# Optimization experiments

Measured on AMD Instinct MI355X. Metric: run time of the kernel, lower is better.

The kernel has to match this reference:

```python
import jax, jax.numpy as jnp
import numpy as np

EPS = 1e-5
HEADS = 4
RES = 28          # resolution H = W
PS = 14           # patch_size (pooled grid side)
POOL = RES // PS  # patch_pool_size = 2


def _local_init_pos_w():
    # Deterministic local init (locality_strength=1.0); kernel_size = sqrt(num_heads) = 2
    ks = int(HEADS ** 0.5)
    center = (ks - 1) / 2 if ks % 2 == 0 else ks // 2
    w = np.zeros((HEADS, 3), dtype=np.float32)
    for h1 in range(ks):
        for h2 in range(ks):
            pos = h1 + ks * h2
            w[pos, 2] = -1.0
            w[pos, 1] = 2.0 * (h1 - center)
            w[pos, 0] = 2.0 * (h2 - center)
    return jnp.asarray(w)


def setup_inputs() -> dict:
    key = jax.random.key(0)
    B, T, C = 32, RES * RES, 768
    x = jax.random.normal(key, (B, T, C), dtype=jnp.float32)
    return {
        "x": x,
        "weight": jnp.ones((C,), jnp.float32),
        "bias": jnp.zeros((C,), jnp.float32),
        "mean_norm_weight": jnp.zeros((HEADS,), jnp.float32),
        "var_norm_weight": jnp.zeros((HEADS,), jnp.float32),
        "pos_w": _local_init_pos_w(),
        "pos_b": jnp.zeros((HEADS,), jnp.float32),
    }


def _rel_indices(ps, dtype):
    # (P, P, 3) relative position features: [indx, indy, indx^2 + indy^2]
    ind = jnp.arange(ps)[None, :] - jnp.arange(ps)[:, None]  # (ps, ps)
    indx = jnp.tile(ind, (ps, ps))                            # (P, P)
    indy = jnp.repeat(jnp.repeat(ind, ps, axis=0), ps, axis=1)
    return jnp.stack([indx, indy, indx * indx + indy * indy], axis=-1).astype(dtype)


def reference(x, weight, bias, mean_norm_weight, var_norm_weight, pos_w, pos_b):
    B, T, C = x.shape
    Ch = C // HEADS
    P = PS * PS

    # group "moment2" normalization
    g = x.reshape(B, T, HEADS, Ch)
    m2 = jnp.mean(g * g, axis=3, keepdims=True)
    xn = (g / jnp.sqrt(m2 + EPS)).reshape(B, T, C)

    mw = jax.nn.sigmoid(mean_norm_weight)  # (HEADS,)
    vw = jax.nn.sigmoid(var_norm_weight)

    # position scores: Linear(3 -> heads) then softmax over source-patch axis
    rel = _rel_indices(PS, x.dtype)                 # (P, P, 3)
    scores = rel @ pos_w.T + pos_b                  # (P, P, HEADS)
    pos = jax.nn.softmax(scores, axis=0)            # softmax over dim -2 of (B,h,i,j)
    pos_h = jnp.transpose(pos, (2, 0, 1))           # (HEADS, P, P)

    mean_ln = xn.mean(axis=2)                       # (B, T)
    var_ln = xn.var(axis=2, ddof=1)                 # torch unbiased var

    # spatialize + avg-pool POOLxPOOL
    xs = xn.reshape(B, RES, RES, C).transpose(0, 3, 1, 2)          # (B, C, 28, 28)
    xp = xs.reshape(B, C, PS, POOL, PS, POOL).mean(axis=(3, 5))    # (B, C, 14, 14)
    xp = xp.reshape(B, HEADS, Ch, P)

    mean_r = jnp.einsum('bhci,hij->bhcj', xp, pos_h)
    mean2_r = jnp.einsum('bhci,hij->bhcj', xp * xp, pos_h)
    var_r = mean2_r - mean_r * mean_r

    def unpool(y):  # nearest-neighbor upsample back to T tokens
        y = y.reshape(B, HEADS, Ch, PS, PS)
        y = jnp.broadcast_to(y[:, :, :, :, None, :, None],
                             (B, HEADS, Ch, PS, POOL, PS, POOL))
        return y.reshape(B, HEADS, Ch, T)

    mean_r = unpool(mean_r)
    var_r = unpool(var_r)

    mwv = mw.reshape(1, HEADS, 1, 1)
    vwv = vw.reshape(1, HEADS, 1, 1)
    mean_r = (1.0 - mwv) * mean_r + mwv * mean_ln[:, None, None, :]
    var_r = (1.0 - vwv) * var_r + vwv * var_ln[:, None, None, :]

    mean_r = mean_r.reshape(B, C, T).transpose(0, 2, 1)  # (B, T, C)
    var_r = var_r.reshape(B, C, T).transpose(0, 2, 1)

    out = (xn - mean_r) / jnp.sqrt(var_r + EPS)
    return out * weight.reshape(1, 1, C) + bias.reshape(1, 1, C)
```

## Files before the change

### kernel.cpp

```cpp
#include <hip/hip_runtime.h>

#define NB   32
#define NT   784
#define NC   768
#define NH   4
#define CH   192
#define PSZ  14
#define NP   196
#define RESO 28
#define EPSV 1e-5f
#define CSL  32
#define NSLC (NC / CSL)
#define BTH  448

__global__ __launch_bounds__(256) void k_norm_pool(
    const float* __restrict__ x,
    float* __restrict__ inv_m2, float* __restrict__ mean_ln,
    float* __restrict__ var_ln, float4* __restrict__ xp4) {
  __shared__ float4 xl4[4 * 192];
  int bid = blockIdx.x;
  int b = bid / NP, ip = bid % NP;
  int pr = ip / PSZ, pc = ip % PSZ;
  int tid = threadIdx.x;
  int k = tid >> 6, lane = tid & 63;
  int t = (2 * pr + (k >> 1)) * RESO + (2 * pc + (k & 1));

  const float4* row = (const float4*)(x + (size_t)(b * NT + t) * NC);
  int f4b = (lane >> 4) * 48 + (lane & 15) * 3;
  float4 v0 = row[f4b], v1 = row[f4b + 1], v2 = row[f4b + 2];

  float d = v0.x * v0.x + v0.y * v0.y + v0.z * v0.z + v0.w * v0.w +
            v1.x * v1.x + v1.y * v1.y + v1.z * v1.z + v1.w * v1.w +
            v2.x * v2.x + v2.y * v2.y + v2.z * v2.z + v2.w * v2.w;
#pragma unroll
  for (int s = 1; s <= 8; s <<= 1) d += __shfl_xor(d, s, 64);
  float iv = rsqrtf(d * (1.f / CH) + EPSV);
  if ((lane & 15) == 0)
    inv_m2[(size_t)(b * NT + t) * NH + (lane >> 4)] = iv;

  v0.x *= iv; v0.y *= iv; v0.z *= iv; v0.w *= iv;
  v1.x *= iv; v1.y *= iv; v1.z *= iv; v1.w *= iv;
  v2.x *= iv; v2.y *= iv; v2.z *= iv; v2.w *= iv;

  float sm = v0.x + v0.y + v0.z + v0.w + v1.x + v1.y + v1.z + v1.w +
             v2.x + v2.y + v2.z + v2.w;
  float sq = v0.x * v0.x + v0.y * v0.y + v0.z * v0.z + v0.w * v0.w +
             v1.x * v1.x + v1.y * v1.y + v1.z * v1.z + v1.w * v1.w +
             v2.x * v2.x + v2.y * v2.y + v2.z * v2.z + v2.w * v2.w;
#pragma unroll
  for (int s = 1; s <= 32; s <<= 1) {
    sm += __shfl_xor(sm, s, 64);
    sq += __shfl_xor(sq, s, 64);
  }
  if (lane == 0) {
    float mean = sm / (float)NC;
    mean_ln[b * NT + t] = mean;
    var_ln[b * NT + t] = (sq - (float)NC * mean * mean) / (float)(NC - 1);
  }

  xl4[k * 192 + f4b]     = v0;
  xl4[k * 192 + f4b + 1] = v1;
  xl4[k * 192 + f4b + 2] = v2;
  __syncthreads();

  if (tid < 192) {
    float4 a = xl4[tid], bb = xl4[192 + tid], c = xl4[384 + tid], dd = xl4[576 + tid];
    float4 r;
    r.x = (a.x + bb.x + c.x + dd.x) * 0.25f;
    r.y = (a.y + bb.y + c.y + dd.y) * 0.25f;
    r.z = (a.z + bb.z + c.z + dd.z) * 0.25f;
    r.w = (a.w + bb.w + c.w + dd.w) * 0.25f;
    xp4[(size_t)(b * NP + ip) * 192 + tid] = r;
  }
}

__global__ __launch_bounds__(BTH) void k_fused(
    const float4* __restrict__ xp4, const float* __restrict__ pos_w,
    const float* __restrict__ mnw, const float* __restrict__ vnw,
    const float* __restrict__ x,
    const float* __restrict__ weight, const float* __restrict__ bias,
    const float* __restrict__ inv_m2, const float* __restrict__ mean_ln,
    const float* __restrict__ var_ln, float* __restrict__ out) {
  __shared__ float4 sxp4[NP * (CSL / 4)];
  __shared__ float sF[PSZ * PSZ];
  __shared__ float sG[PSZ * PSZ];
  __shared__ float tstat[NT][3];

  int bid0 = blockIdx.x;
  int bidS = (bid0 & 7) * 96 + (bid0 >> 3);
  int b = bidS / NSLC, s = bidS % NSLC;
  int hs = s / 6;
  int tid = threadIdx.x;
  int jx = tid >> 5;
  int ch = tid & 31;
  int c = s * CSL + ch;

  if (tid < PSZ) {
    int jf = tid;
    float w0 = pos_w[hs * 3 + 0], w2 = pos_w[hs * 3 + 2];
    float e[PSZ], mx = -1e30f;
#pragma unroll
    for (int i = 0; i < PSZ; ++i) {
      float dd = (float)(jf - i);
      float sc = w0 * dd + w2 * dd * dd;
      e[i] = sc; mx = fmaxf(mx, sc);
    }
    float sum = 0.f;
#pragma unroll
    for (int i = 0; i < PSZ; ++i) { e[i] = expf(e[i] - mx); sum += e[i]; }
    float invs = 1.f / sum;
#pragma unroll
    for (int i = 0; i < PSZ; ++i) sF[jf * PSZ + i] = e[i] * invs;
  }
  if (tid >= 64 && tid < 64 + PSZ) {
    int jr = tid - 64;
    float w1 = pos_w[hs * 3 + 1], w2 = pos_w[hs * 3 + 2];
    float e[PSZ], mx = -1e30f;
#pragma unroll
    for (int i = 0; i < PSZ; ++i) {
      float dd = (float)(jr - i);
      float sc = w1 * dd + w2 * dd * dd;
      e[i] = sc; mx = fmaxf(mx, sc);
    }
    float sum = 0.f;
#pragma unroll
    for (int i = 0; i < PSZ; ++i) { e[i] = expf(e[i] - mx); sum += e[i]; }
    float invs = 1.f / sum;
#pragma unroll
    for (int i = 0; i < PSZ; ++i) sG[jr * PSZ + i] = e[i] * invs;
  }

  {
    const float4* src = xp4 + (size_t)b * NP * (NC / 4) + s * (CSL / 4);
    for (int i = tid; i < NP * (CSL / 4); i += BTH) {
      int p = i >> 3, q = i & 7;
      sxp4[i] = src[(size_t)p * (NC / 4) + q];
    }
  }
  for (int i = tid; i < NT; i += BTH) {
    size_t o = (size_t)(b * NT + i);
    tstat[i][0] = inv_m2[o * NH + hs];
    tstat[i][1] = mean_ln[o];
    tstat[i][2] = var_ln[o];
  }

  float mw = 1.f / (1.f + expf(-mnw[hs]));
  float vw = 1.f / (1.f + expf(-vnw[hs]));
  float omw = 1.f - mw, ovw = 1.f - vw;
  float wv = weight[c], bv = bias[c];

  __syncthreads();

  float t1[PSZ], t2[PSZ];
#pragma unroll
  for (int iy = 0; iy < PSZ; ++iy) { t1[iy] = 0.f; t2[iy] = 0.f; }

  const float* sx = (const float*)sxp4;
#pragma unroll
  for (int iy = 0; iy < PSZ; ++iy) {
#pragma unroll
    for (int ix = 0; ix < PSZ; ++ix) {
      float f = sF[jx * PSZ + ix];
      float v = sx[(iy * PSZ + ix) * CSL + ch];
      t1[iy] += f * v;
      t2[iy] += f * (v * v);
    }
  }

#pragma unroll 1
  for (int jy = 0; jy < PSZ; ++jy) {
    float m = 0.f, q = 0.f;
#pragma unroll
    for (int iy = 0; iy < PSZ; ++iy) {
      float g = sG[jy * PSZ + iy];
      m += g * t1[iy];
      q += g * t2[iy];
    }
    float p = fmaxf(q - m * m, 0.f);
    float mb = omw * m, vb = ovw * p;

#pragma unroll
    for (int kk = 0; kk < 4; ++kk) {
      int t = (2 * jy + (kk >> 1)) * RESO + (2 * jx + (kk & 1));
      size_t xo = (size_t)(b * NT + t) * NC + c;
      float ivv = tstat[t][0];
      float ml  = tstat[t][1], vl = tstat[t][2];

      float xn = x[xo] * ivv;
      float mr = mb + mw * ml;
      float vr = vb + vw * vl;
      out[xo] = (xn - mr) * rsqrtf(vr + EPSV) * wv + bv;
    }
  }
}

extern "C" void kernel_launch(void* const* d_in, const int* in_sizes, int n_in,
                              void* d_out, int out_size, void* d_ws, size_t ws_size,
                              hipStream_t stream) {
  const float* x     = (const float*)d_in[0];
  const float* wgt   = (const float*)d_in[1];
  const float* bias  = (const float*)d_in[2];
  const float* mnw   = (const float*)d_in[3];
  const float* vnw   = (const float*)d_in[4];
  const float* pos_w = (const float*)d_in[5];
  float* out = (float*)d_out;

  float* ws      = (float*)d_ws;
  float* inv_m2  = ws;
  float* mean_ln = inv_m2 + (size_t)NB * NT * NH;
  float* var_ln  = mean_ln + (size_t)NB * NT;
  float* xp      = var_ln + (size_t)NB * NT;

  hipLaunchKernelGGL(k_norm_pool, dim3(NB * NP), dim3(256), 0, stream,
                     x, inv_m2, mean_ln, var_ln, (float4*)xp);
  hipLaunchKernelGGL(k_fused, dim3(NB * NSLC), dim3(BTH), 0, stream,
                     (const float4*)xp, pos_w, mnw, vnw, x, wgt, bias,
                     inv_m2, mean_ln, var_ln, out);
}
```

Before: 168.5 us.

## Stage pooled stats through LDS to emit float4 vectorized output stores

The final output phase of the fused kernel is restructured. Each chunk of two pooled rows writes its per-channel mean and variance terms into shared memory, reusing the pooled-input buffer. A remapped thread layout then reads x and writes out as float4 across all 28 token columns. This replaces scalar 4-byte loads and stores that covered 128 bytes per token row, and the weight and bias are now staged in shared memory. The cost is extra __syncthreads barriers per chunk and shared-memory round trips.

```diff
diff --git a/kernel.cpp b/kernel.cpp
--- a/kernel.cpp
+++ b/kernel.cpp
@@ -77,14 +77,15 @@
 __global__ __launch_bounds__(BTH) void k_fused(
     const float4* __restrict__ xp4, const float* __restrict__ pos_w,
     const float* __restrict__ mnw, const float* __restrict__ vnw,
-    const float* __restrict__ x,
-    const float* __restrict__ weight, const float* __restrict__ bias,
+    const float4* __restrict__ x4,
+    const float4* __restrict__ weight4, const float4* __restrict__ bias4,
     const float* __restrict__ inv_m2, const float* __restrict__ mean_ln,
-    const float* __restrict__ var_ln, float* __restrict__ out) {
+    const float* __restrict__ var_ln, float4* __restrict__ out4) {
   __shared__ float4 sxp4[NP * (CSL / 4)];
   __shared__ float sF[PSZ * PSZ];
   __shared__ float sG[PSZ * PSZ];
   __shared__ float tstat[NT][3];
+  __shared__ float4 sWB[2][CSL / 4];
 
   int bid0 = blockIdx.x;
   int bidS = (bid0 & 7) * 96 + (bid0 >> 3);
@@ -93,7 +94,6 @@
   int tid = threadIdx.x;
   int jx = tid >> 5;
   int ch = tid & 31;
-  int c = s * CSL + ch;
 
   if (tid < PSZ) {
     int jf = tid;
@@ -128,6 +128,12 @@
     float invs = 1.f / sum;
 #pragma unroll
     for (int i = 0; i < PSZ; ++i) sG[jr * PSZ + i] = e[i] * invs;
+  }
+  if (tid >= 128 && tid < 128 + CSL / 4) {
+    sWB[0][tid - 128] = weight4[s * (CSL / 4) + (tid - 128)];
+  }
+  if (tid >= 160 && tid < 160 + CSL / 4) {
+    sWB[1][tid - 160] = bias4[s * (CSL / 4) + (tid - 160)];
   }
 
   {
@@ -147,7 +153,6 @@
   float mw = 1.f / (1.f + expf(-mnw[hs]));
   float vw = 1.f / (1.f + expf(-vnw[hs]));
   float omw = 1.f - mw, ovw = 1.f - vw;
-  float wv = weight[c], bv = bias[c];
 
   __syncthreads();
 
@@ -166,31 +171,56 @@
       t2[iy] += f * (v * v);
     }
   }
+  __syncthreads();
+
+  float* smv = (float*)sxp4;
+  const float4* xb = x4 + (size_t)b * NT * (NC / 4) + s * (CSL / 4);
+  float4* ob = out4 + (size_t)b * NT * (NC / 4) + s * (CSL / 4);
 
 #pragma unroll 1
-  for (int jy = 0; jy < PSZ; ++jy) {
-    float m = 0.f, q = 0.f;
-#pragma unroll
-    for (int iy = 0; iy < PSZ; ++iy) {
-      float g = sG[jy * PSZ + iy];
-      m += g * t1[iy];
-      q += g * t2[iy];
-    }
-    float p = fmaxf(q - m * m, 0.f);
-    float mb = omw * m, vb = ovw * p;
-
-#pragma unroll
-    for (int kk = 0; kk < 4; ++kk) {
-      int t = (2 * jy + (kk >> 1)) * RESO + (2 * jx + (kk & 1));
-      size_t xo = (size_t)(b * NT + t) * NC + c;
+  for (int chunk = 0; chunk < 7; ++chunk) {
+#pragma unroll
+    for (int jyl = 0; jyl < 2; ++jyl) {
+      int jy = chunk * 2 + jyl;
+      float m = 0.f, q = 0.f;
+#pragma unroll
+      for (int iy = 0; iy < PSZ; ++iy) {
+        float g = sG[jy * PSZ + iy];
+        m += g * t1[iy];
+        q += g * t2[iy];
+      }
+      float p = fmaxf(q - m * m, 0.f);
+      smv[(jyl * PSZ + jx) * CSL + ch]            = omw * m;
+      smv[((2 + jyl) * PSZ + jx) * CSL + ch]      = ovw * p;
+    }
+    __syncthreads();
+
+#pragma unroll
+    for (int k = 0; k < 2; ++k) {
+      int w = tid + BTH * k;
+      int slot = w & 7;
+      int r2 = w >> 3;
+      int tcol = r2 % 28, trl = r2 / 28;
+      int trow = chunk * 4 + trl;
+      int t = trow * RESO + tcol;
+      int jyl = trl >> 1, jx2 = tcol >> 1;
+
+      float4 mb4 = *(const float4*)&smv[(jyl * PSZ + jx2) * CSL + slot * 4];
+      float4 vb4 = *(const float4*)&smv[((2 + jyl) * PSZ + jx2) * CSL + slot * 4];
       float ivv = tstat[t][0];
-      float ml  = tstat[t][1], vl = tstat[t][2];
-
-      float xn = x[xo] * ivv;
-      float mr = mb + mw * ml;
-      float vr = vb + vw * vl;
-      out[xo] = (xn - mr) * rsqrtf(vr + EPSV) * wv + bv;
-    }
+      float mr = mw * tstat[t][1];
+      float vr = vw * tstat[t][2] + EPSV;
+      float4 wv = sWB[0][slot], bv = sWB[1][slot];
+
+      float4 xv = xb[(size_t)t * (NC / 4) + slot];
+      float4 r;
+      r.x = (xv.x * ivv - (mb4.x + mr)) * rsqrtf(vb4.x + vr) * wv.x + bv.x;
+      r.y = (xv.y * ivv - (mb4.y + mr)) * rsqrtf(vb4.y + vr) * wv.y + bv.y;
+      r.z = (xv.z * ivv - (mb4.z + mr)) * rsqrtf(vb4.z + vr) * wv.z + bv.z;
+      r.w = (xv.w * ivv - (mb4.w + mr)) * rsqrtf(vb4.w + vr) * wv.w + bv.w;
+      ob[(size_t)t * (NC / 4) + slot] = r;
+    }
+    __syncthreads();
   }
 }
 
@@ -214,6 +244,7 @@
   hipLaunchKernelGGL(k_norm_pool, dim3(NB * NP), dim3(256), 0, stream,
                      x, inv_m2, mean_ln, var_ln, (float4*)xp);
   hipLaunchKernelGGL(k_fused, dim3(NB * NSLC), dim3(BTH), 0, stream,
-                     (const float4*)xp, pos_w, mnw, vnw, x, wgt, bias,
-                     inv_m2, mean_ln, var_ln, out);
+                     (const float4*)xp, pos_w, mnw, vnw, (const float4*)x,
+                     (const float4*)wgt, (const float4*)bias,
+                     inv_m2, mean_ln, var_ln, (float4*)out);
 }
```

New measurement: 165.1 us. 1.02x faster.
